# Kernel tuning notes

Hardware: AMD Instinct MI355X
Metric: run time of the kernel (lower is better)

The kernel has to match this reference:

```python
import jax, jax.numpy as jnp
import numpy as np

EMBED_DIM = 768
NUM_HEADS = 12
HEAD_DIM = EMBED_DIM // NUM_HEADS
WINDOW = 64
B, S = 2, 2048


def setup_inputs() -> dict:
    key = jax.random.key(0)
    ks = jax.random.split(key, 8)
    xavier = 0.1 * np.sqrt(6.0 / (EMBED_DIM + EMBED_DIM))  # xavier_uniform with gain=0.1
    def lin_w(k):
        return jax.random.uniform(k, (EMBED_DIM, EMBED_DIM), jnp.float32, -xavier, xavier)
    return {
        "query": jax.random.normal(ks[0], (B, S, EMBED_DIM), jnp.float32),
        "key": jax.random.normal(ks[1], (B, S, EMBED_DIM), jnp.float32),
        "value": jax.random.normal(ks[2], (B, S, EMBED_DIM), jnp.float32),
        "key_padding_mask": jnp.zeros((B, S), dtype=bool),
        "Wq": lin_w(ks[3]), "bq": jnp.zeros((EMBED_DIM,), jnp.float32),
        "Wk": lin_w(ks[4]), "bk": jnp.zeros((EMBED_DIM,), jnp.float32),
        "Wv": lin_w(ks[5]), "bv": jnp.zeros((EMBED_DIM,), jnp.float32),
        "Wo": lin_w(ks[6]), "bo": jnp.zeros((EMBED_DIM,), jnp.float32),
    }


def reference(query, key, value, key_padding_mask, Wq, bq, Wk, bk, Wv, bv, Wo, bo):
    Bsz, Sl, E = query.shape
    H, D = NUM_HEADS, HEAD_DIM

    def proj(x, W, b):  # nn.Linear: x @ W.T + b, then split heads -> [B,H,S,D]
        return (x @ W.T + b).reshape(Bsz, Sl, H, D).transpose(0, 2, 1, 3)

    q = proj(query, Wq, bq)
    k = proj(key, Wk, bk)
    v = proj(value, Wv, bv)

    scale = float(D) ** -0.5
    scores = jnp.einsum("bhqd,bhkd->bhqk", q, k) * scale  # [B,H,S,S]

    idx = jnp.arange(Sl)
    win_mask = jnp.abs(idx[:, None] - idx[None, :]) > WINDOW  # True = masked out
    scores = jnp.where(win_mask[None, None], -10000.0, scores)
    scores = jnp.where(key_padding_mask[:, None, None, :], -10000.0, scores)
    scores = jnp.where(jnp.isnan(scores), -10000.0, scores)

    attn = jax.nn.softmax(scores, axis=-1) + 1e-6
    attn = jnp.where(jnp.isnan(attn), 1.0 / Sl, attn)

    ctx = jnp.einsum("bhqk,bhkd->bhqd", attn, v)
    ctx = ctx.transpose(0, 2, 1, 3).reshape(Bsz, Sl, E)
    out = ctx @ Wo.T + bo
    out = jnp.where(jnp.isnan(out), value, out)
    return out, attn
```

## Files before the change

### kernel.cpp

```cpp
#include <hip/hip_runtime.h>
#include <hip/hip_bf16.h>

#define EMBED 768
#define NHEADS 12
#define HDIM 64
#define WIN 64
#define BATCH 2
#define SEQ 2048
#define MROWS (BATCH*SEQ)
#define NBH (BATCH*NHEADS)
#define QT 32
#define KP 160
#define KPAD 168
#define SPAD 164

typedef __attribute__((ext_vector_type(8))) short short8;
typedef __attribute__((ext_vector_type(4))) float f32x4;

__device__ __forceinline__ float bf2f(unsigned short u) {
    union { unsigned int i; float f; } z;
    z.i = ((unsigned int)u) << 16;
    return z.f;
}
__device__ __forceinline__ unsigned short f2bf(float f) {
    __hip_bfloat16 h = __float2bfloat16(f);
    return *reinterpret_cast<unsigned short*>(&h);
}

__device__ __forceinline__ void gload16(const unsigned short* g, unsigned short* l) {
    __builtin_amdgcn_global_load_lds(
        (const __attribute__((address_space(1))) unsigned int*)g,
        (__attribute__((address_space(3))) unsigned int*)l,
        16, 0, 0);
}

struct CvtArgs {
    const float* src[7];
    unsigned short* dst[7];
    int n4[7];
    int bstart[8];
};

__global__ __launch_bounds__(256) void cvt_all(CvtArgs ca) {
    int bid = blockIdx.x;
    int seg = 0;
#pragma unroll
    for (int s = 0; s < 6; ++s)
        if (bid >= ca.bstart[s + 1]) seg = s + 1;
    int i = (bid - ca.bstart[seg]) * 256 + threadIdx.x;
    if (i < ca.n4[seg]) {
        float4 v = reinterpret_cast<const float4*>(ca.src[seg])[i];
        ushort4 o;
        o.x = f2bf(v.x); o.y = f2bf(v.y); o.z = f2bf(v.z); o.w = f2bf(v.w);
        reinterpret_cast<ushort4*>(ca.dst[seg])[i] = o;
    }
}

struct GArgs {
    const unsigned short* A[3];
    const unsigned short* Bm[3];
    const float* bias[3];
    void* C[3];
};

template<int F32OUT>
__global__ __launch_bounds__(256) void gemm_nt(GArgs ga, int M, int N, int K) {
    const int z = blockIdx.z;
    const unsigned short* __restrict__ A  = ga.A[z];
    const unsigned short* __restrict__ Bm = ga.Bm[z];
    const float* __restrict__ bias = ga.bias[z];

    const int bm = blockIdx.y * 128;
    const int bn = blockIdx.x * 128;

    __shared__ unsigned short As[128 * 32];
    __shared__ unsigned short Bs[128 * 32];

    const int tid = threadIdx.x;
    const int lane = tid & 63;
    const int wid = tid >> 6;
    const int wm = wid >> 1, wn = wid & 1;

    f32x4 acc[4][4] = {};

    const int fr = lane & 15;
    const int krow = (lane >> 4) * 8;

    for (int k0 = 0; k0 < K; k0 += 32) {
#pragma unroll
        for (int it = 0; it < 2; ++it) {
            int idx = it * 256 + tid;
            int r = idx >> 2;
            int c = (idx & 3) * 8;
            gload16(A + (size_t)(bm + r) * K + k0 + c, &As[idx * 8]);
            gload16(Bm + (size_t)(bn + r) * K + k0 + c, &Bs[idx * 8]);
        }
        __syncthreads();

        short8 af[4], bfv[4];
#pragma unroll
        for (int mf = 0; mf < 4; ++mf)
            af[mf] = *reinterpret_cast<const short8*>(&As[(wm * 64 + mf * 16 + fr) * 32 + krow]);
#pragma unroll
        for (int nf = 0; nf < 4; ++nf)
            bfv[nf] = *reinterpret_cast<const short8*>(&Bs[(wn * 64 + nf * 16 + fr) * 32 + krow]);
#pragma unroll
        for (int mf = 0; mf < 4; ++mf)
#pragma unroll
            for (int nf = 0; nf < 4; ++nf)
                acc[mf][nf] = __builtin_amdgcn_mfma_f32_16x16x32_bf16(
                    af[mf], bfv[nf], acc[mf][nf], 0, 0, 0);
        __syncthreads();
    }

    const int fq = lane >> 4;
#pragma unroll
    for (int mf = 0; mf < 4; ++mf)
#pragma unroll
        for (int nf = 0; nf < 4; ++nf) {
            int col = bn + wn * 64 + nf * 16 + fr;
            float bv = bias[col];
#pragma unroll
            for (int r = 0; r < 4; ++r) {
                int row = bm + wm * 64 + mf * 16 + fq * 4 + r;
                float v = acc[mf][nf][r] + bv;
                if (F32OUT)
                    reinterpret_cast<float*>(ga.C[z])[(size_t)row * N + col] = v;
                else
                    reinterpret_cast<unsigned short*>(ga.C[z])[(size_t)row * N + col] = f2bf(v);
            }
        }
}

__global__ __launch_bounds__(256) void sumv_kernel(const unsigned short* __restrict__ Vb,
                                                   float* __restrict__ sumV) {
    __shared__ float r[32][HDIM];
    const int bh = blockIdx.x;
    const int b = bh / NHEADS, h = bh % NHEADS;
    const int dg = (threadIdx.x & 7) * 8;
    const int r0 = threadIdx.x >> 3;
    float acc[8] = {};
    const unsigned short* vp = Vb + (size_t)(b * SEQ) * EMBED + h * HDIM + dg;
    for (int j = r0; j < SEQ; j += 32) {
        short8 v = *reinterpret_cast<const short8*>(vp + (size_t)j * EMBED);
#pragma unroll
        for (int e = 0; e < 8; ++e)
            acc[e] += bf2f(((const unsigned short*)&v)[e]);
    }
#pragma unroll
    for (int e = 0; e < 8; ++e) r[r0][dg + e] = acc[e];
    __syncthreads();
    if (threadIdx.x < HDIM) {
        float s = 0.f;
#pragma unroll
        for (int i = 0; i < 32; ++i) s += r[i][threadIdx.x];
        sumV[bh * HDIM + threadIdx.x] = s;
    }
}

__global__ __launch_bounds__(256, 3) void attn_mfma(
    const unsigned short* __restrict__ Q,
    const unsigned short* __restrict__ Kb,
    const unsigned short* __restrict__ Vb,
    const unsigned char* __restrict__ kpm,
    const float* __restrict__ sumV,
    float* __restrict__ attn_out,
    unsigned short* __restrict__ ctx) {
    const int qt = blockIdx.x;
    const int bh = blockIdx.y;
    const int h = bh % NHEADS;
    const int b = bh / NHEADS;
    const int q0 = qt * QT;
    const int kstart = max(q0 - WIN, 0);

    __shared__ float Sf[QT][SPAD];
    __shared__ unsigned short Pb[QT][KPAD];
    __shared__ unsigned short Vt[HDIM][KPAD];

    const int tid = threadIdx.x;
    const int l = tid & 63;
    const int w = tid >> 6;
    const int fr = l & 15;
    const int ksl = (l >> 4) * 8;

    const size_t base = (size_t)(b * SEQ) * EMBED + h * HDIM;

    {
        const int mf = w >> 1;
        const int nt0 = (w & 1) * 5;

        const unsigned short* qrow = Q + base + (size_t)(q0 + mf * 16 + fr) * EMBED;
        short8 aq0 = *reinterpret_cast<const short8*>(qrow + ksl);
        short8 aq1 = *reinterpret_cast<const short8*>(qrow + 32 + ksl);

        f32x4 sacc[5] = {};
#pragma unroll
        for (int t = 0; t < 5; ++t) {
            int jg = kstart + (nt0 + t) * 16 + fr;
            int jc = min(jg, SEQ - 1);
            const unsigned short* krow = Kb + base + (size_t)jc * EMBED;
            short8 b0 = *reinterpret_cast<const short8*>(krow + ksl);
            short8 b1 = *reinterpret_cast<const short8*>(krow + 32 + ksl);
            sacc[t] = __builtin_amdgcn_mfma_f32_16x16x32_bf16(aq0, b0, sacc[t], 0, 0, 0);
            sacc[t] = __builtin_amdgcn_mfma_f32_16x16x32_bf16(aq1, b1, sacc[t], 0, 0, 0);
        }

#pragma unroll
        for (int t = 0; t < 5; ++t) {
            int col = (nt0 + t) * 16 + fr;
            int jg = kstart + col;
            bool jvalid = (jg < SEQ);
            bool mk = jvalid && kpm[b * SEQ + jg];
#pragma unroll
            for (int r = 0; r < 4; ++r) {
                int rowl = mf * 16 + (l >> 4) * 4 + r;
                int qi = q0 + rowl;
                float s = sacc[t][r] * 0.125f;
                if (mk) s = -10000.f;
                int dd = qi - jg;
                if (!jvalid || dd > WIN || dd < -WIN) s = -1e30f;
                Sf[rowl][col] = s;
            }
        }

#pragma unroll
        for (int pass = 0; pass < 5; ++pass) {
            int jrel = pass * 32 + (tid >> 3);
            int jg = kstart + jrel;
            int dg = (tid & 7) * 8;
            short8 v = {};
            if (jg < SEQ)
                v = *reinterpret_cast<const short8*>(Vb + base + (size_t)jg * EMBED + dg);
#pragma unroll
            for (int e = 0; e < 8; ++e)
                Vt[dg + e][jrel] = ((const unsigned short*)&v)[e];
        }
    }
    __syncthreads();

    {
        const int row = tid >> 3;
        const int cg = tid & 7;
        float e[KP / 8];
        float m = -1e30f;
#pragma unroll
        for (int i = 0; i < KP / 8; ++i) {
            float s = Sf[row][cg + i * 8];
            e[i] = s;
            m = fmaxf(m, s);
        }
#pragma unroll
        for (int off = 1; off < 8; off <<= 1) m = fmaxf(m, __shfl_xor(m, off));
        float sum = 0.f;
#pragma unroll
        for (int i = 0; i < KP / 8; ++i) {
            e[i] = __expf(e[i] - m);
            sum += e[i];
        }
#pragma unroll
        for (int off = 1; off < 8; off <<= 1) sum += __shfl_xor(sum, off);
        float inv = 1.f / sum;
#pragma unroll
        for (int i = 0; i < KP / 8; ++i) {
            float p = e[i] * inv;
            int col = cg + i * 8;
            Sf[row][col] = p;
            Pb[row][col] = f2bf(p);
        }
    }
    __syncthreads();

    {
#pragma unroll
        for (int rr = 0; rr < QT / 4; ++rr) {
            int row = w * (QT / 4) + rr;
            int qi = q0 + row;
            int blo = max(qi - WIN, 0);
            int bhi = min(qi + WIN, SEQ - 1);
            float* __restrict__ orow = attn_out + ((size_t)bh * SEQ + qi) * SEQ;
#pragma unroll
            for (int seg = 0; seg < SEQ / 256; ++seg) {
                int c0 = seg * 256 + l * 4;
                f32x4 v = {1e-6f, 1e-6f, 1e-6f, 1e-6f};
                if (c0 + 3 >= blo && c0 <= bhi) {
#pragma unroll
                    for (int e = 0; e < 4; ++e) {
                        int c = c0 + e;
                        if (c >= blo && c <= bhi) v[e] = Sf[row][c - kstart] + 1e-6f;
                    }
                }
                __builtin_nontemporal_store(v, reinterpret_cast<f32x4*>(orow + c0));
            }
        }
    }

    {
        const int mf = w >> 1;
        const int nfb = (w & 1) * 2;
        f32x4 oacc[2] = {};
#pragma unroll
        for (int kk = 0; kk < KP / 32; ++kk) {
            short8 a = *reinterpret_cast<const short8*>(&Pb[mf * 16 + fr][kk * 32 + ksl]);
#pragma unroll
            for (int n2 = 0; n2 < 2; ++n2) {
                short8 bv = *reinterpret_cast<const short8*>(&Vt[(nfb + n2) * 16 + fr][kk * 32 + ksl]);
                oacc[n2] = __builtin_amdgcn_mfma_f32_16x16x32_bf16(a, bv, oacc[n2], 0, 0, 0);
            }
        }
#pragma unroll
        for (int n2 = 0; n2 < 2; ++n2) {
            int d = (nfb + n2) * 16 + fr;
            float sv = 1e-6f * sumV[bh * HDIM + d];
#pragma unroll
            for (int r = 0; r < 4; ++r) {
                int rowl = mf * 16 + (l >> 4) * 4 + r;
                ctx[base + (size_t)(q0 + rowl) * EMBED + d] = f2bf(oacc[n2][r] + sv);
            }
        }
    }
}

extern "C" void kernel_launch(void* const* d_in, const int* in_sizes, int n_in,
                              void* d_out, int out_size, void* d_ws, size_t ws_size,
                              hipStream_t stream) {
    const float* q_in = (const float*)d_in[0];
    const float* k_in = (const float*)d_in[1];
    const float* v_in = (const float*)d_in[2];
    const unsigned char* kpm = (const unsigned char*)d_in[3];
    const float* Wq = (const float*)d_in[4];
    const float* bq = (const float*)d_in[5];
    const float* Wk = (const float*)d_in[6];
    const float* bk = (const float*)d_in[7];
    const float* Wv = (const float*)d_in[8];
    const float* bv = (const float*)d_in[9];
    const float* Wo = (const float*)d_in[10];
    const float* bo = (const float*)d_in[11];

    char* ws = (char*)d_ws;
    size_t off = 0;
    auto alloc = [&](size_t bytes) {
        void* p = ws + off;
        off += (bytes + 255) & ~255ULL;
        return p;
    };
    const size_t XB = (size_t)MROWS * EMBED * 2;
    const size_t WB = (size_t)EMBED * EMBED * 2;
    unsigned short* xq = (unsigned short*)alloc(XB);
    unsigned short* xk = (unsigned short*)alloc(XB);
    unsigned short* xv = (unsigned short*)alloc(XB);
    unsigned short* wqb = (unsigned short*)alloc(WB);
    unsigned short* wkb = (unsigned short*)alloc(WB);
    unsigned short* wvb = (unsigned short*)alloc(WB);
    unsigned short* wob = (unsigned short*)alloc(WB);
    unsigned short* Qb = (unsigned short*)alloc(XB);
    unsigned short* Kb = (unsigned short*)alloc(XB);
    unsigned short* Vb = (unsigned short*)alloc(XB);
    unsigned short* ctx = (unsigned short*)alloc(XB);
    float* sumV = (float*)alloc((size_t)NBH * HDIM * 4);

    float* out0 = (float*)d_out;
    float* attn_out = out0 + (size_t)MROWS * EMBED;

    {
        CvtArgs ca;
        const float* srcs[7] = {q_in, k_in, v_in, Wq, Wk, Wv, Wo};
        unsigned short* dsts[7] = {xq, xk, xv, wqb, wkb, wvb, wob};
        int bacc = 0;
        for (int s = 0; s < 7; ++s) {
            ca.src[s] = srcs[s];
            ca.dst[s] = dsts[s];
            ca.n4[s] = (s < 3) ? (MROWS * EMBED / 4) : (EMBED * EMBED / 4);
            ca.bstart[s] = bacc;
            bacc += (ca.n4[s] + 255) / 256;
        }
        ca.bstart[7] = bacc;
        cvt_all<<<dim3(bacc), dim3(256), 0, stream>>>(ca);
    }

    {
        GArgs ga;
        ga.A[0] = xq;  ga.A[1] = xk;  ga.A[2] = xv;
        ga.Bm[0] = wqb; ga.Bm[1] = wkb; ga.Bm[2] = wvb;
        ga.bias[0] = bq; ga.bias[1] = bk; ga.bias[2] = bv;
        ga.C[0] = Qb; ga.C[1] = Kb; ga.C[2] = Vb;
        gemm_nt<0><<<dim3(EMBED / 128, MROWS / 128, 3), dim3(256), 0, stream>>>(
            ga, MROWS, EMBED, EMBED);
    }

    sumv_kernel<<<dim3(NBH), dim3(256), 0, stream>>>(Vb, sumV);

    attn_mfma<<<dim3(SEQ / QT, NBH), dim3(256), 0, stream>>>(
        Qb, Kb, Vb, kpm, sumV, attn_out, ctx);

    {
        GArgs ga;
        ga.A[0] = ctx;  ga.A[1] = ctx;  ga.A[2] = ctx;
        ga.Bm[0] = wob; ga.Bm[1] = wob; ga.Bm[2] = wob;
        ga.bias[0] = bo; ga.bias[1] = bo; ga.bias[2] = bo;
        ga.C[0] = out0; ga.C[1] = out0; ga.C[2] = out0;
        gemm_nt<1><<<dim3(EMBED / 128, MROWS / 128, 1), dim3(256), 0, stream>>>(
            ga, MROWS, EMBED, EMBED);
    }
}
```

Measured before the change: 176.8 us.

## Move constant attn-matrix fill into QKV GEMM to overlap with compute

The attention kernel now writes only the 256-column segments near the diagonal of each attention row. The QKV projection GEMM, which is compute-bound, takes over the constant 1e-6 fill of all other segments, spread across its waves in each K iteration. The aim is to hide the large memory-bound store of the attention output behind MFMA work. In exchange the GEMM gets extra store traffic and index arithmetic, and correctness now depends on the fill mapping covering exactly the segments the attention kernel skips.

```diff
diff --git a/kernel.cpp b/kernel.cpp
--- a/kernel.cpp
+++ b/kernel.cpp
@@ -13,6 +13,8 @@
 #define KP 160
 #define KPAD 168
 #define SPAD 164
+#define NWAVES_QKV 2304
+#define FILL_PER_WAVE 128
 
 typedef __attribute__((ext_vector_type(8))) short short8;
 typedef __attribute__((ext_vector_type(4))) float f32x4;
@@ -61,9 +63,10 @@
     const unsigned short* Bm[3];
     const float* bias[3];
     void* C[3];
+    float* fill_out;
 };
 
-template<int F32OUT>
+template<int F32OUT, int FILLER>
 __global__ __launch_bounds__(256) void gemm_nt(GArgs ga, int M, int N, int K) {
     const int z = blockIdx.z;
     const unsigned short* __restrict__ A  = ga.A[z];
@@ -80,6 +83,8 @@
     const int lane = tid & 63;
     const int wid = tid >> 6;
     const int wm = wid >> 1, wn = wid & 1;
+
+    const int gwave = (((blockIdx.z * gridDim.y) + blockIdx.y) * gridDim.x + blockIdx.x) * 4 + wid;
 
     f32x4 acc[4][4] = {};
 
@@ -96,6 +101,29 @@
             gload16(Bm + (size_t)(bn + r) * K + k0 + c, &Bs[idx * 8]);
         }
         __syncthreads();
+
+        if (FILLER) {
+            const f32x4 fillv = {1e-6f, 1e-6f, 1e-6f, 1e-6f};
+            int t = k0 >> 5;
+#pragma unroll
+            for (int s = 0; s < 6; ++s) {
+                int item_idx = t * 6 + s;
+                if (item_idx < FILL_PER_WAVE) {
+                    int item = gwave + item_idx * NWAVES_QKV;
+                    int row = item / 6;
+                    int slot = item - row * 6;
+                    int qi = row & (SEQ - 1);
+                    int c = qi >> 8;
+                    int nN = (c == 0 || c == 7) ? 2 : 3;
+                    int thr = (c - 1 > 0) ? c - 1 : 0;
+                    int seg = slot + ((slot >= thr) ? nN : 0);
+                    if (seg < 8)
+                        __builtin_nontemporal_store(fillv,
+                            reinterpret_cast<f32x4*>(
+                                ga.fill_out + (size_t)row * SEQ + seg * 256 + lane * 4));
+                }
+            }
+        }
 
         short8 af[4], bfv[4];
 #pragma unroll
@@ -277,16 +305,18 @@
             int qi = q0 + row;
             int blo = max(qi - WIN, 0);
             int bhi = min(qi + WIN, SEQ - 1);
+            int c = qi >> 8;
+            int slo = max(c - 1, 0);
+            int shi = min(c + 1, 7);
             float* __restrict__ orow = attn_out + ((size_t)bh * SEQ + qi) * SEQ;
-#pragma unroll
-            for (int seg = 0; seg < SEQ / 256; ++seg) {
+            for (int seg = slo; seg <= shi; ++seg) {
                 int c0 = seg * 256 + l * 4;
                 f32x4 v = {1e-6f, 1e-6f, 1e-6f, 1e-6f};
                 if (c0 + 3 >= blo && c0 <= bhi) {
 #pragma unroll
                     for (int e = 0; e < 4; ++e) {
-                        int c = c0 + e;
-                        if (c >= blo && c <= bhi) v[e] = Sf[row][c - kstart] + 1e-6f;
+                        int cc = c0 + e;
+                        if (cc >= blo && cc <= bhi) v[e] = Sf[row][cc - kstart] + 1e-6f;
                     }
                 }
                 __builtin_nontemporal_store(v, reinterpret_cast<f32x4*>(orow + c0));
@@ -383,7 +413,8 @@
         ga.Bm[0] = wqb; ga.Bm[1] = wkb; ga.Bm[2] = wvb;
         ga.bias[0] = bq; ga.bias[1] = bk; ga.bias[2] = bv;
         ga.C[0] = Qb; ga.C[1] = Kb; ga.C[2] = Vb;
-        gemm_nt<0><<<dim3(EMBED / 128, MROWS / 128, 3), dim3(256), 0, stream>>>(
+        ga.fill_out = attn_out;
+        gemm_nt<0, 1><<<dim3(EMBED / 128, MROWS / 128, 3), dim3(256), 0, stream>>>(
             ga, MROWS, EMBED, EMBED);
     }
 
@@ -398,7 +429,8 @@
         ga.Bm[0] = wob; ga.Bm[1] = wob; ga.Bm[2] = wob;
         ga.bias[0] = bo; ga.bias[1] = bo; ga.bias[2] = bo;
         ga.C[0] = out0; ga.C[1] = out0; ga.C[2] = out0;
-        gemm_nt<1><<<dim3(EMBED / 128, MROWS / 128, 1), dim3(256), 0, stream>>>(
+        ga.fill_out = nullptr;
+        gemm_nt<1, 0><<<dim3(EMBED / 128, MROWS / 128, 1), dim3(256), 0, stream>>>(
             ga, MROWS, EMBED, EMBED);
     }
 }
```

Result: no change. 179.4 us (+1.5%).
